# Kernel optimization log

Hardware: AMD Instinct MI355X
Metric: run time of the kernel (lower is better)

The kernel has to match this reference:

```python
import jax, jax.numpy as jnp
import numpy as np

S, B, D, H = 2048, 4, 1024, 16
DK = D // H  # 64


def setup_inputs() -> dict:
    key = jax.random.key(0)
    ks = jax.random.split(key, 11)
    scale = 1.0 / np.sqrt(D)  # xavier-ish init scale
    return {
        "queries": jax.random.normal(ks[0], (S, B, D), jnp.float32),
        "keys": jax.random.normal(ks[1], (S, B, D), jnp.float32),
        "values": jax.random.normal(ks[2], (S, B, D), jnp.float32),
        # torch Linear weights: [out_features, in_features], y = x @ W.T + b
        "Wq": jax.random.normal(ks[3], (D, D), jnp.float32) * scale,
        "bq": jnp.zeros((D,), jnp.float32),
        "Wk": jax.random.normal(ks[4], (D, D), jnp.float32) * scale,
        "bk": jnp.zeros((D,), jnp.float32),
        "Wv": jax.random.normal(ks[5], (D, D), jnp.float32) * scale,
        "bv": jnp.zeros((D,), jnp.float32),
        "Wo": jax.random.normal(ks[6], (D, D), jnp.float32) * scale,
        "bo": jnp.zeros((D,), jnp.float32),
    }


def reference(queries, keys, values, Wq, bq, Wk, bk, Wv, bv, Wo, bo):
    # inputs are seq-first [S, B, D]; module permutes to batch-first
    q_in = jnp.transpose(queries, (1, 0, 2))  # [B, S, D]
    k_in = jnp.transpose(keys, (1, 0, 2))
    v_in = jnp.transpose(values, (1, 0, 2))
    b_s, nq, _ = q_in.shape
    nk = k_in.shape[1]

    # groups=1: grouped view is a no-op -> plain Linear projections
    q = (q_in @ Wq.T + bq).reshape(b_s, nq, H, DK)  # [B, Sq, H, DK]
    k = (k_in @ Wk.T + bk).reshape(b_s, nk, H, DK)
    v = (v_in @ Wv.T + bv).reshape(b_s, nk, H, DK)

    # scores [B, H, Sq, Sk], scaled by 1/sqrt(d_k)
    att = jnp.einsum("bqhd,bkhd->bhqk", q, k) / np.sqrt(DK).astype(np.float32)
    att = jax.nn.softmax(att, axis=-1)
    # dropout p=0.0 (eval semantics): identity

    out = jnp.einsum("bhqk,bkhd->bqhd", att, v).reshape(b_s, nq, H * DK)
    out = out @ Wo.T + bo  # [B, Sq, D]
    return jnp.transpose(out, (1, 0, 2))  # back to [S, B, D]
```

## Files before the change

### kernel.cpp

```cpp
#include <hip/hip_runtime.h>
#include <stdint.h>

#define S_LEN 2048
#define NB    4
#define DMOD  1024
#define NH    16
#define HD    64

typedef float f32x4 __attribute__((ext_vector_type(4)));
typedef float f32x16 __attribute__((ext_vector_type(16)));
typedef short bf16x8 __attribute__((ext_vector_type(8)));
typedef unsigned int u32x4 __attribute__((ext_vector_type(4)));
typedef unsigned short u16;
typedef unsigned int u32;

__device__ __forceinline__ u16 f32_to_bf16(float f) {
  union { float f; unsigned int u; } v; v.f = f;
  unsigned int r = v.u + 0x7fffu + ((v.u >> 16) & 1u);
  return (u16)(r >> 16);
}

__device__ __forceinline__ float fast_exp2(float x) {
#if __has_builtin(__builtin_amdgcn_exp2f)
  return __builtin_amdgcn_exp2f(x);
#else
  return exp2f(x);
#endif
}

typedef __attribute__((address_space(1))) const unsigned int gu32;
typedef __attribute__((address_space(3))) unsigned int lu32;
__device__ __forceinline__ void async_copy16(const void* g, void* l) {
  __builtin_amdgcn_global_load_lds((gu32*)g, (lu32*)l, 16, 0, 0);
}

__global__ __launch_bounds__(256) void convert_all(
    const float* __restrict__ w0, const float* __restrict__ w1,
    const float* __restrict__ w2, const float* __restrict__ w3,
    const float* __restrict__ x0, const float* __restrict__ x1,
    const float* __restrict__ x2,
    u16* __restrict__ o0, u16* __restrict__ o1, u16* __restrict__ o2,
    u16* __restrict__ o3, u16* __restrict__ o4, u16* __restrict__ o5,
    u16* __restrict__ o6) {
  const float* in; u16* out; int n;
  switch (blockIdx.y) {
    case 0: in = w0; out = o0; n = 1 << 20; break;
    case 1: in = w1; out = o1; n = 1 << 20; break;
    case 2: in = w2; out = o2; n = 1 << 20; break;
    case 3: in = w3; out = o3; n = 1 << 20; break;
    case 4: in = x0; out = o4; n = 1 << 23; break;
    case 5: in = x1; out = o5; n = 1 << 23; break;
    default: in = x2; out = o6; n = 1 << 23; break;
  }
  for (int i = (blockIdx.x * 256 + threadIdx.x) * 4; i < n; i += gridDim.x * 1024) {
    float4 v = *(const float4*)(in + i);
    ushort4 o;
    o.x = f32_to_bf16(v.x); o.y = f32_to_bf16(v.y);
    o.z = f32_to_bf16(v.z); o.w = f32_to_bf16(v.w);
    *(ushort4*)(out + i) = o;
  }
}

__global__ __launch_bounds__(256) void gemm_proj(
    const u16* __restrict__ Xqb, const u16* __restrict__ Xkb, const u16* __restrict__ Xvb,
    const u16* __restrict__ Wqb, const u16* __restrict__ Wkb, const u16* __restrict__ Wvb,
    const float* __restrict__ bq, const float* __restrict__ bk, const float* __restrict__ bv,
    u16* __restrict__ Qo, u16* __restrict__ Ko, u16* __restrict__ Vo, float qscale) {
  __shared__ u16 a_lds[128 * 32];
  __shared__ u16 b_lds[128 * 32];
  const int lin = blockIdx.x + (blockIdx.y << 6) + (blockIdx.z << 9);
  const int c   = lin & 7;
  const int idx = lin >> 3;
  const int which = idx >> 6;
  const int t   = idx & 63;
  const int m0 = (c * 8 + (t >> 3)) * 128;
  const int n0 = (t & 7) * 128;

  const u16* A  = (which == 0) ? Xqb : (which == 1) ? Xkb : Xvb;
  const u16* Bw = (which == 0) ? Wqb : (which == 1) ? Wkb : Wvb;
  const float* bias = (which == 0) ? bq : (which == 1) ? bk : bv;

  const int tid  = threadIdx.x;
  const int wid  = tid >> 6;
  const int lane = tid & 63;
  const int wm = wid >> 1, wn = wid & 1;

  f32x4 acc[4][4] = {};

  for (int kt = 0; kt < 32; ++kt) {
    const int k0 = kt * 32;
    __syncthreads();
    #pragma unroll
    for (int i = 0; i < 2; ++i) {
      int row = wid * 32 + i * 16 + (lane >> 2);
      int sc  = (lane & 3) ^ ((row >> 1) & 3);
      async_copy16(Bw + (size_t)(n0 + row) * 1024 + k0 + sc * 8, b_lds + wid * 1024 + i * 512);
      async_copy16(A + (size_t)(m0 + row) * 1024 + k0 + sc * 8, a_lds + wid * 1024 + i * 512);
    }
    asm volatile("s_waitcnt vmcnt(0)" ::: "memory");
    __syncthreads();

    bf16x8 af[4], bfr[4];
    #pragma unroll
    for (int mi = 0; mi < 4; ++mi) {
      int row = wm * 64 + mi * 16 + (lane & 15);
      int ch  = (lane >> 4) ^ ((row >> 1) & 3);
      af[mi] = *(const bf16x8*)(a_lds + row * 32 + ch * 8);
    }
    #pragma unroll
    for (int ni = 0; ni < 4; ++ni) {
      int row = wn * 64 + ni * 16 + (lane & 15);
      int ch  = (lane >> 4) ^ ((row >> 1) & 3);
      bfr[ni] = *(const bf16x8*)(b_lds + row * 32 + ch * 8);
    }
    #pragma unroll
    for (int mi = 0; mi < 4; ++mi)
      #pragma unroll
      for (int ni = 0; ni < 4; ++ni)
        acc[mi][ni] = __builtin_amdgcn_mfma_f32_16x16x32_bf16(af[mi], bfr[ni], acc[mi][ni], 0, 0, 0);
  }

  #pragma unroll
  for (int ni = 0; ni < 4; ++ni) {
    int n = n0 + wn * 64 + ni * 16 + (lane & 15);
    float bv = bias[n];
    int hh = n >> 6, dk = n & 63;
    #pragma unroll
    for (int mi = 0; mi < 4; ++mi) {
      int sbase = m0 + wm * 64 + mi * 16 + ((lane >> 4) << 2);
      int s = sbase >> 2;
      if (which == 0) {
        #pragma unroll
        for (int r = 0; r < 4; ++r)
          Qo[((size_t)(r * NH + hh) * S_LEN + s) * HD + dk] =
              f32_to_bf16((acc[mi][ni][r] + bv) * qscale);
      } else if (which == 1) {
        int dkp = (((dk >> 2) ^ (s & 15)) << 2) | (dk & 3);
        #pragma unroll
        for (int r = 0; r < 4; ++r)
          Ko[((size_t)(r * NH + hh) * S_LEN + s) * HD + dkp] =
              f32_to_bf16(acc[mi][ni][r] + bv);
      } else {
        int sp = (s & ~63) | ((((s >> 2) & 15) ^ (dk & 15)) << 2) | (s & 3);
        #pragma unroll
        for (int r = 0; r < 4; ++r)
          Vo[((size_t)(r * NH + hh) * HD + dk) * S_LEN + sp] =
              f32_to_bf16(acc[mi][ni][r] + bv);
      }
    }
  }
}

__global__ __launch_bounds__(256) void gemm_out(const u16* __restrict__ Ab,
                                                const u16* __restrict__ Bw,
                                                const float* __restrict__ bias,
                                                float* __restrict__ outp) {
  __shared__ u16 a_lds[128 * 64];
  __shared__ u16 b_lds[128 * 64];
  const int lin = blockIdx.x + (blockIdx.y << 6);
  const int c   = lin & 7;
  const int idx = lin >> 3;
  const int m0 = (c * 8 + (idx >> 3)) * 128;
  const int n0 = (idx & 7) * 128;
  const int tid  = threadIdx.x;
  const int wid  = tid >> 6;
  const int lane = tid & 63;
  const int wm = wid >> 1, wn = wid & 1;

  f32x4 acc[4][4] = {};

  for (int kt = 0; kt < 16; ++kt) {
    const int k0 = kt * 64;
    __syncthreads();
    #pragma unroll
    for (int j = 0; j < 4; ++j) {
      int row = wid * 32 + j * 8 + (lane >> 3);
      int sc  = (lane & 7) ^ (row & 7);
      async_copy16(Bw + (size_t)(n0 + row) * 1024 + k0 + sc * 8,
                   b_lds + (wid * 32 + j * 8) * 64);
      async_copy16(Ab + (size_t)(m0 + row) * 1024 + k0 + sc * 8,
                   a_lds + (wid * 32 + j * 8) * 64);
    }
    asm volatile("s_waitcnt vmcnt(0)" ::: "memory");
    __syncthreads();

    #pragma unroll
    for (int s32 = 0; s32 < 2; ++s32) {
      bf16x8 af[4], bfr[4];
      #pragma unroll
      for (int mi = 0; mi < 4; ++mi) {
        int row = wm * 64 + mi * 16 + (lane & 15);
        int ch  = (s32 * 4 + (lane >> 4)) ^ (row & 7);
        af[mi] = *(const bf16x8*)(a_lds + row * 64 + ch * 8);
      }
      #pragma unroll
      for (int ni = 0; ni < 4; ++ni) {
        int row = wn * 64 + ni * 16 + (lane & 15);
        int ch  = (s32 * 4 + (lane >> 4)) ^ (row & 7);
        bfr[ni] = *(const bf16x8*)(b_lds + row * 64 + ch * 8);
      }
      #pragma unroll
      for (int mi = 0; mi < 4; ++mi)
        #pragma unroll
        for (int ni = 0; ni < 4; ++ni)
          acc[mi][ni] = __builtin_amdgcn_mfma_f32_16x16x32_bf16(af[mi], bfr[ni], acc[mi][ni], 0, 0, 0);
    }
  }

  #pragma unroll
  for (int ni = 0; ni < 4; ++ni) {
    int n = n0 + wn * 64 + ni * 16 + (lane & 15);
    float bv = bias[n];
    #pragma unroll
    for (int mi = 0; mi < 4; ++mi) {
      int sbase = m0 + wm * 64 + mi * 16 + ((lane >> 4) << 2);
      #pragma unroll
      for (int r = 0; r < 4; ++r) {
        int m = sbase + r;
        int bb = m >> 11, s = m & 2047;
        outp[((size_t)(s * NB + bb)) * 1024 + n] = acc[mi][ni][r] + bv;
      }
    }
  }
}

__global__ __launch_bounds__(512, 4) void attn_kernel(const u16* __restrict__ Qb,
                                                      const u16* __restrict__ Kb,
                                                      const u16* __restrict__ Vt,
                                                      u16* __restrict__ Oatt) {
  __shared__ u16 kbuf[2][64 * 64];
  __shared__ u16 vbuf[2][64 * 64];
  __shared__ float alds[8][32];
  const int tid = threadIdx.x;
  const int w = tid >> 6, lane = tid & 63;
  const int hi = lane >> 5, l31 = lane & 31;
  const int lin = blockIdx.x;
  const int bh = (lin & 7) + 8 * (lin >> 6);
  const int qt = (lin >> 3) & 7;
  const int h = bh & 15, b = bh >> 4;
  const int q0 = qt * 256 + w * 32;
  const int key = l31 & 15;

  bf16x8 qf[4];
  {
    const u16* qp = Qb + ((size_t)bh * S_LEN + q0 + l31) * HD + hi * 8;
    #pragma unroll
    for (int s = 0; s < 4; ++s) qf[s] = *(const bf16x8*)(qp + s * 16);
  }

  f32x16 acc0 = {}, acc1 = {};
  float l_run = 0.0f;

  const int rl = w * 8 + (lane >> 3);
  const u16* ksrc = Kb + ((size_t)bh * S_LEN + rl) * HD + (lane & 7) * 8;
  const u16* vsrc = Vt + ((size_t)bh * HD + rl) * S_LEN + (lane & 7) * 8;

  async_copy16(ksrc, &kbuf[0][w * 512]);
  async_copy16(vsrc, &vbuf[0][w * 512]);
  asm volatile("s_waitcnt vmcnt(0)" ::: "memory");
  __syncthreads();

  for (int kb = 0; kb < 32; ++kb) {
    const int cur = kb & 1;
    if (kb + 1 < 32) {
      async_copy16(ksrc + (size_t)(kb + 1) * 64 * HD, &kbuf[cur ^ 1][w * 512]);
      async_copy16(vsrc + (kb + 1) * 64, &vbuf[cur ^ 1][w * 512]);
    }
    const u16* KL = kbuf[cur];
    const u16* VL = vbuf[cur];

    f32x16 pk0 = {}, pk1 = {};
    __builtin_amdgcn_s_setprio(1);
    #pragma unroll
    for (int s = 0; s < 4; ++s) {
      const int c0 = 4 * s + 2 * hi;
      const int p0 = (c0 ^ key) * 4;
      const int p1 = ((c0 + 1) ^ key) * 4;
      uint2 a0 = *(const uint2*)(KL + l31 * 64 + p0);
      uint2 a1 = *(const uint2*)(KL + l31 * 64 + p1);
      uint2 b0 = *(const uint2*)(KL + (32 + l31) * 64 + p0);
      uint2 b1 = *(const uint2*)(KL + (32 + l31) * 64 + p1);
      u32x4 kw0 = {a0.x, a0.y, a1.x, a1.y};
      u32x4 kw1 = {b0.x, b0.y, b1.x, b1.y};
      pk0 = __builtin_amdgcn_mfma_f32_32x32x16_bf16(__builtin_bit_cast(bf16x8, kw0), qf[s], pk0, 0, 0, 0);
      pk1 = __builtin_amdgcn_mfma_f32_32x32x16_bf16(__builtin_bit_cast(bf16x8, kw1), qf[s], pk1, 0, 0, 0);
    }
    __builtin_amdgcn_s_setprio(0);

    #pragma unroll
    for (int r = 0; r < 16; ++r) {
      pk0[r] = fast_exp2(pk0[r]);
      pk1[r] = fast_exp2(pk1[r]);
    }

    {
      float t16[16];
      #pragma unroll
      for (int r = 0; r < 16; ++r) t16[r] = pk0[r] + pk1[r];
      float t8[8];
      #pragma unroll
      for (int r = 0; r < 8; ++r) t8[r] = t16[r] + t16[r + 8];
      float t4[4];
      #pragma unroll
      for (int r = 0; r < 4; ++r) t4[r] = t8[r] + t8[r + 4];
      float rs = (t4[0] + t4[1]) + (t4[2] + t4[3]);
#if __has_builtin(__builtin_amdgcn_permlane32_swap)
      u32 ru = __builtin_bit_cast(u32, rs);
      auto sw = __builtin_amdgcn_permlane32_swap(ru, ru, false, false);
      rs += __builtin_bit_cast(float, hi ? sw[0] : sw[1]);
#else
      rs += __shfl_xor(rs, 32);
#endif
      l_run += rs;
    }

    u32 c0v[8], c1v[8];
    #pragma unroll
    for (int i = 0; i < 8; ++i) {
      float a0 = pk0[2 * i], b0 = pk0[2 * i + 1];
      float a1 = pk1[2 * i], b1 = pk1[2 * i + 1];
      asm("v_cvt_pk_bf16_f32 %0, %1, %2" : "=v"(c0v[i]) : "v"(a0), "v"(b0));
      asm("v_cvt_pk_bf16_f32 %0, %1, %2" : "=v"(c1v[i]) : "v"(a1), "v"(b1));
    }

    __builtin_amdgcn_s_setprio(1);
    #pragma unroll
    for (int g = 0; g < 2; ++g) {
      u32 pa0[4], pa1[4];
#if __has_builtin(__builtin_amdgcn_permlane32_swap)
      {
        auto s0 = __builtin_amdgcn_permlane32_swap(c0v[4*g+0], c0v[4*g+2], false, false);
        auto s1 = __builtin_amdgcn_permlane32_swap(c0v[4*g+1], c0v[4*g+3], false, false);
        pa0[0] = s0[0]; pa0[2] = s0[1]; pa0[1] = s1[0]; pa0[3] = s1[1];
        auto t0 = __builtin_amdgcn_permlane32_swap(c1v[4*g+0], c1v[4*g+2], false, false);
        auto t1 = __builtin_amdgcn_permlane32_swap(c1v[4*g+1], c1v[4*g+3], false, false);
        pa1[0] = t0[0]; pa1[2] = t0[1]; pa1[1] = t1[0]; pa1[3] = t1[1];
      }
#else
      {
        u32 x0 = c0v[4*g+0], x1 = c0v[4*g+1], y0 = c0v[4*g+2], y1 = c0v[4*g+3];
        u32 X0 = __shfl_xor((int)x0, 32), X1 = __shfl_xor((int)x1, 32);
        u32 Y0 = __shfl_xor((int)y0, 32), Y1 = __shfl_xor((int)y1, 32);
        pa0[0] = hi ? Y0 : x0; pa0[1] = hi ? Y1 : x1;
        pa0[2] = hi ? y0 : X0; pa0[3] = hi ? y1 : X1;
        x0 = c1v[4*g+0]; x1 = c1v[4*g+1]; y0 = c1v[4*g+2]; y1 = c1v[4*g+3];
        X0 = __shfl_xor((int)x0, 32); X1 = __shfl_xor((int)x1, 32);
        Y0 = __shfl_xor((int)y0, 32); Y1 = __shfl_xor((int)y1, 32);
        pa1[0] = hi ? Y0 : x0; pa1[1] = hi ? Y1 : x1;
        pa1[2] = hi ? y0 : X0; pa1[3] = hi ? y1 : X1;
      }
#endif
      #pragma unroll
      for (int t = 0; t < 2; ++t) {
        const int ks = t == 0 ? g : 2 + g;
        u32x4 pw = t == 0 ? (u32x4){pa0[0], pa0[1], pa0[2], pa0[3]}
                          : (u32x4){pa1[0], pa1[1], pa1[2], pa1[3]};
        bf16x8 paf = __builtin_bit_cast(bf16x8, pw);
        const int c0c = 4 * ks + 2 * hi;
        const int p0 = (c0c ^ key) * 4;
        const int p1 = ((c0c + 1) ^ key) * 4;
        uint2 va0 = *(const uint2*)(VL + l31 * 64 + p0);
        uint2 va1 = *(const uint2*)(VL + l31 * 64 + p1);
        uint2 vb0 = *(const uint2*)(VL + (32 + l31) * 64 + p0);
        uint2 vb1 = *(const uint2*)(VL + (32 + l31) * 64 + p1);
        u32x4 vw0 = {va0.x, va0.y, va1.x, va1.y};
        u32x4 vw1 = {vb0.x, vb0.y, vb1.x, vb1.y};
        acc0 = __builtin_amdgcn_mfma_f32_32x32x16_bf16(paf, __builtin_bit_cast(bf16x8, vw0), acc0, 0, 0, 0);
        acc1 = __builtin_amdgcn_mfma_f32_32x32x16_bf16(paf, __builtin_bit_cast(bf16x8, vw1), acc1, 0, 0, 0);
      }
    }
    __builtin_amdgcn_s_setprio(0);

    asm volatile("s_waitcnt vmcnt(0)" ::: "memory");
    __syncthreads();
  }

  if (lane < 32) alds[w][l31] = l_run;
  #pragma unroll
  for (int r = 0; r < 16; ++r) {
    const int crow = (r & 3) + 8 * (r >> 2) + 4 * hi;
    const int q = q0 + crow;
    u16* op = Oatt + ((size_t)b * S_LEN + q) * DMOD + h * HD;
    const float inv = 1.0f / alds[w][crow];
    op[l31]      = f32_to_bf16(acc0[r] * inv);
    op[32 + l31] = f32_to_bf16(acc1[r] * inv);
  }
}

extern "C" void kernel_launch(void* const* d_in, const int* in_sizes, int n_in,
                              void* d_out, int out_size, void* d_ws, size_t ws_size,
                              hipStream_t stream) {
  const float* Xq = (const float*)d_in[0];
  const float* Xk = (const float*)d_in[1];
  const float* Xv = (const float*)d_in[2];
  const float* Wq = (const float*)d_in[3];
  const float* bq = (const float*)d_in[4];
  const float* Wk = (const float*)d_in[5];
  const float* bk = (const float*)d_in[6];
  const float* Wv = (const float*)d_in[7];
  const float* bv = (const float*)d_in[8];
  const float* Wo = (const float*)d_in[9];
  const float* bo = (const float*)d_in[10];

  u16* Wqb = (u16*)d_ws;
  u16* Wkb = Wqb + (1 << 20);
  u16* Wvb = Wkb + (1 << 20);
  u16* Wob = Wvb + (1 << 20);
  u16* Qb  = Wob + (1 << 20);
  const size_t QKV = (size_t)64 * S_LEN * HD;
  u16* Kb  = Qb + QKV;
  u16* Vt  = Kb + QKV;
  u16* Oat = Vt + QKV;
  u16* Xqb = Oat + QKV;
  u16* Xkb = Xqb + QKV;
  u16* Xvb = Xkb + QKV;

  convert_all<<<dim3(2048, 7), 256, 0, stream>>>(Wq, Wk, Wv, Wo, Xq, Xk, Xv,
                                                 Wqb, Wkb, Wvb, Wob, Xqb, Xkb, Xvb);

  gemm_proj<<<dim3(64, 8, 3), 256, 0, stream>>>(Xqb, Xkb, Xvb, Wqb, Wkb, Wvb,
                                                bq, bk, bv, Qb, Kb, Vt,
                                                0.125f * 1.4426950408889634f);

  attn_kernel<<<dim3(512), 512, 0, stream>>>(Qb, Kb, Vt, Oat);

  gemm_out<<<dim3(64, 8), 256, 0, stream>>>(Oat, Wob, bo, (float*)d_out);
}
```

Before: 210.7 us.

## Fuse fp32-to-bf16 activation conversion into projection GEMM A-tile loads

The separate pass that converted the three fp32 activation tensors to bf16 is removed. The projection GEMM now loads fp32 A tiles with register loads, converts them in-register and writes swizzled bf16 to LDS, while B tiles still use async global-to-LDS copies. The conversion kernel now handles only the weights. The block-to-tile mapping is also reshuffled. This removes a full write and reread of bf16 activations, but A loads become synchronous register loads that read twice the bytes and are reread by each of the 8 N-tiles.

```diff
diff --git a/kernel.cpp b/kernel.cpp
--- a/kernel.cpp
+++ b/kernel.cpp
@@ -34,50 +34,45 @@
   __builtin_amdgcn_global_load_lds((gu32*)g, (lu32*)l, 16, 0, 0);
 }
 
-__global__ __launch_bounds__(256) void convert_all(
+__global__ __launch_bounds__(256) void convert4_kernel(
     const float* __restrict__ w0, const float* __restrict__ w1,
     const float* __restrict__ w2, const float* __restrict__ w3,
-    const float* __restrict__ x0, const float* __restrict__ x1,
-    const float* __restrict__ x2,
-    u16* __restrict__ o0, u16* __restrict__ o1, u16* __restrict__ o2,
-    u16* __restrict__ o3, u16* __restrict__ o4, u16* __restrict__ o5,
-    u16* __restrict__ o6) {
-  const float* in; u16* out; int n;
+    u16* __restrict__ o0, u16* __restrict__ o1,
+    u16* __restrict__ o2, u16* __restrict__ o3) {
+  const float* in; u16* out;
   switch (blockIdx.y) {
-    case 0: in = w0; out = o0; n = 1 << 20; break;
-    case 1: in = w1; out = o1; n = 1 << 20; break;
-    case 2: in = w2; out = o2; n = 1 << 20; break;
-    case 3: in = w3; out = o3; n = 1 << 20; break;
-    case 4: in = x0; out = o4; n = 1 << 23; break;
-    case 5: in = x1; out = o5; n = 1 << 23; break;
-    default: in = x2; out = o6; n = 1 << 23; break;
-  }
-  for (int i = (blockIdx.x * 256 + threadIdx.x) * 4; i < n; i += gridDim.x * 1024) {
-    float4 v = *(const float4*)(in + i);
-    ushort4 o;
-    o.x = f32_to_bf16(v.x); o.y = f32_to_bf16(v.y);
-    o.z = f32_to_bf16(v.z); o.w = f32_to_bf16(v.w);
-    *(ushort4*)(out + i) = o;
-  }
+    case 0: in = w0; out = o0; break;
+    case 1: in = w1; out = o1; break;
+    case 2: in = w2; out = o2; break;
+    default: in = w3; out = o3; break;
+  }
+  int i = (blockIdx.x * 256 + threadIdx.x) * 4;
+  float4 v = *(const float4*)(in + i);
+  ushort4 o;
+  o.x = f32_to_bf16(v.x); o.y = f32_to_bf16(v.y);
+  o.z = f32_to_bf16(v.z); o.w = f32_to_bf16(v.w);
+  *(ushort4*)(out + i) = o;
 }
 
 __global__ __launch_bounds__(256) void gemm_proj(
-    const u16* __restrict__ Xqb, const u16* __restrict__ Xkb, const u16* __restrict__ Xvb,
+    const float* __restrict__ Xq, const float* __restrict__ Xk, const float* __restrict__ Xv,
     const u16* __restrict__ Wqb, const u16* __restrict__ Wkb, const u16* __restrict__ Wvb,
     const float* __restrict__ bq, const float* __restrict__ bk, const float* __restrict__ bv,
     u16* __restrict__ Qo, u16* __restrict__ Ko, u16* __restrict__ Vo, float qscale) {
   __shared__ u16 a_lds[128 * 32];
   __shared__ u16 b_lds[128 * 32];
   const int lin = blockIdx.x + (blockIdx.y << 6) + (blockIdx.z << 9);
-  const int c   = lin & 7;
-  const int idx = lin >> 3;
+  const int c    = lin & 7;
+  const int idx  = lin >> 3;
   const int which = idx >> 6;
-  const int t   = idx & 63;
-  const int m0 = (c * 8 + (t >> 3)) * 128;
-  const int n0 = (t & 7) * 128;
-
-  const u16* A  = (which == 0) ? Xqb : (which == 1) ? Xkb : Xvb;
-  const u16* Bw = (which == 0) ? Wqb : (which == 1) ? Wkb : Wvb;
+  const int r6   = idx & 63;
+  const int half = r6 >> 5;
+  const int w32  = r6 & 31;
+  const int m0 = (((half << 3) + c) * 4 + (w32 >> 3)) * 128;
+  const int n0 = (w32 & 7) * 128;
+
+  const float* A  = (which == 0) ? Xq : (which == 1) ? Xk : Xv;
+  const u16* Bw   = (which == 0) ? Wqb : (which == 1) ? Wkb : Wvb;
   const float* bias = (which == 0) ? bq : (which == 1) ? bk : bv;
 
   const int tid  = threadIdx.x;
@@ -85,18 +80,47 @@
   const int lane = tid & 63;
   const int wm = wid >> 1, wn = wid & 1;
 
+  const int arow  = tid >> 1, ahalf = tid & 1;
+  const float* Ap = A + (size_t)(m0 + arow) * 1024 + ahalf * 16;
+  const int akey  = (arow >> 1) & 3;
+  const int slot0 = (ahalf * 2 + 0) ^ akey;
+  const int slot1 = (ahalf * 2 + 1) ^ akey;
+  u16* awr = a_lds + arow * 32;
+
+  const int srow0 = wid * 32 + (lane >> 2);
+  const int srow1 = srow0 + 16;
+  const int sc0 = (lane & 3) ^ ((srow0 >> 1) & 3);
+  const int sc1 = (lane & 3) ^ ((srow1 >> 1) & 3);
+  const u16* Bp0 = Bw + (size_t)(n0 + srow0) * 1024 + sc0 * 8;
+  const u16* Bp1 = Bw + (size_t)(n0 + srow1) * 1024 + sc1 * 8;
+
   f32x4 acc[4][4] = {};
 
   for (int kt = 0; kt < 32; ++kt) {
     const int k0 = kt * 32;
     __syncthreads();
-    #pragma unroll
-    for (int i = 0; i < 2; ++i) {
-      int row = wid * 32 + i * 16 + (lane >> 2);
-      int sc  = (lane & 3) ^ ((row >> 1) & 3);
-      async_copy16(Bw + (size_t)(n0 + row) * 1024 + k0 + sc * 8, b_lds + wid * 1024 + i * 512);
-      async_copy16(A + (size_t)(m0 + row) * 1024 + k0 + sc * 8, a_lds + wid * 1024 + i * 512);
-    }
+
+    async_copy16(Bp0 + k0, b_lds + wid * 1024);
+    async_copy16(Bp1 + k0, b_lds + wid * 1024 + 512);
+
+    {
+      float4 av0 = *(const float4*)(Ap + k0 + 0);
+      float4 av1 = *(const float4*)(Ap + k0 + 4);
+      float4 av2 = *(const float4*)(Ap + k0 + 8);
+      float4 av3 = *(const float4*)(Ap + k0 + 12);
+      u16 tmp[16];
+      tmp[0]  = f32_to_bf16(av0.x); tmp[1]  = f32_to_bf16(av0.y);
+      tmp[2]  = f32_to_bf16(av0.z); tmp[3]  = f32_to_bf16(av0.w);
+      tmp[4]  = f32_to_bf16(av1.x); tmp[5]  = f32_to_bf16(av1.y);
+      tmp[6]  = f32_to_bf16(av1.z); tmp[7]  = f32_to_bf16(av1.w);
+      tmp[8]  = f32_to_bf16(av2.x); tmp[9]  = f32_to_bf16(av2.y);
+      tmp[10] = f32_to_bf16(av2.z); tmp[11] = f32_to_bf16(av2.w);
+      tmp[12] = f32_to_bf16(av3.x); tmp[13] = f32_to_bf16(av3.y);
+      tmp[14] = f32_to_bf16(av3.z); tmp[15] = f32_to_bf16(av3.w);
+      *(int4*)(awr + slot0 * 8) = *(const int4*)(tmp + 0);
+      *(int4*)(awr + slot1 * 8) = *(const int4*)(tmp + 8);
+    }
+
     asm volatile("s_waitcnt vmcnt(0)" ::: "memory");
     __syncthreads();
 
@@ -411,14 +435,10 @@
   u16* Kb  = Qb + QKV;
   u16* Vt  = Kb + QKV;
   u16* Oat = Vt + QKV;
-  u16* Xqb = Oat + QKV;
-  u16* Xkb = Xqb + QKV;
-  u16* Xvb = Xkb + QKV;
-
-  convert_all<<<dim3(2048, 7), 256, 0, stream>>>(Wq, Wk, Wv, Wo, Xq, Xk, Xv,
-                                                 Wqb, Wkb, Wvb, Wob, Xqb, Xkb, Xvb);
-
-  gemm_proj<<<dim3(64, 8, 3), 256, 0, stream>>>(Xqb, Xkb, Xvb, Wqb, Wkb, Wvb,
+
+  convert4_kernel<<<dim3(1024, 4), 256, 0, stream>>>(Wq, Wk, Wv, Wo, Wqb, Wkb, Wvb, Wob);
+
+  gemm_proj<<<dim3(64, 8, 3), 256, 0, stream>>>(Xq, Xk, Xv, Wqb, Wkb, Wvb,
                                                 bq, bk, bv, Qb, Kb, Vt,
                                                 0.125f * 1.4426950408889634f);
 
```

Result: no change. 208.0 us (median of 2 runs) (-1.3%).
